# Performance work log

Measured on AMD Instinct MI355X. Metric: run time of the kernel, lower is better.

The kernel has to match this reference:

```python
import jax, jax.numpy as jnp
import numpy as np

EMBED_DIM = 768
NUM_HEADS = 12
HEAD_DIM = EMBED_DIM // NUM_HEADS
BS, SEQ = 2, 2048
NEG_BIG = -1e20  # matches torch masked_fill value


def setup_inputs() -> dict:
    key = jax.random.key(0)
    ks = jax.random.split(key, 8)
    Q = jax.random.normal(ks[0], (BS, SEQ, EMBED_DIM), dtype=jnp.float32)
    K = jax.random.normal(ks[1], (BS, SEQ, EMBED_DIM), dtype=jnp.float32)
    V = jax.random.normal(ks[2], (BS, SEQ, EMBED_DIM), dtype=jnp.float32)
    mask = jax.random.randint(ks[3], (1, 1, SEQ, SEQ), 0, 2, dtype=jnp.int32)
    scale = 1.0 / np.sqrt(EMBED_DIM).astype(np.float32)
    Wq = jax.random.normal(ks[4], (EMBED_DIM, EMBED_DIM), dtype=jnp.float32) * 0.02
    Wk = jax.random.normal(ks[5], (EMBED_DIM, EMBED_DIM), dtype=jnp.float32) * 0.02
    Wv = jax.random.normal(ks[6], (EMBED_DIM, EMBED_DIM), dtype=jnp.float32) * 0.02
    Wo = jax.random.normal(ks[7], (EMBED_DIM, EMBED_DIM), dtype=jnp.float32) * 0.02
    return {"Q": Q, "K": K, "V": V, "mask": mask,
            "Wq": Wq, "Wk": Wk, "Wv": Wv, "Wo": Wo}


def reference(Q, K, V, mask, Wq, Wk, Wv, Wo):
    bs, q_len, D = Q.shape
    H, hd = NUM_HEADS, HEAD_DIM
    # QKV projections (nn.Linear, no bias): x @ W.T
    q = (Q @ Wq.T).reshape(bs, q_len, H, hd)            # nqhd
    k = (K @ Wk.T).reshape(bs, K.shape[1], H, hd)       # nkhd
    v = (V @ Wv.T).reshape(bs, V.shape[1], H, hd)       # nlhd
    # unfused attention, faithful to source (scale by sqrt(embed_dim)!)
    energy = jnp.einsum('nqhd,nkhd->nhqk', q, k)
    energy = jnp.where(mask == 0, jnp.float32(NEG_BIG), energy)
    attn = jax.nn.softmax(energy * (1.0 / jnp.sqrt(jnp.float32(D))), axis=3)
    out = jnp.einsum('nhql,nlhd->nqhd', attn, v).reshape(bs, q_len, H * hd)
    return out @ Wo.T
```

## Files before the change

kernel.cpp:

```cpp
#include <hip/hip_runtime.h>
#include <cmath>

typedef __bf16 bf16x8 __attribute__((ext_vector_type(8)));
typedef float f32x4 __attribute__((ext_vector_type(4)));
typedef unsigned int u32x4 __attribute__((ext_vector_type(4)));

#define SEQ 2048
#define EMBED 768
#define NHEAD 12
#define HDIM 64
#define NTOK 4096
#define NBH 24
#define NSPLIT 2
#define TILES_PER_SPLIT (SEQ / 64 / NSPLIT)
#define SCALE_LOG2 (1.4426950408889634f * 0.036084391824351615f)

__device__ __forceinline__ void gload_lds16(const __bf16* g, __bf16* l) {
  __builtin_amdgcn_global_load_lds(
      (const __attribute__((address_space(1))) void*)g,
      (__attribute__((address_space(3))) void*)l, 16, 0, 0);
}

__device__ __forceinline__ unsigned pack2(float a, float b) {
  unsigned short lo = __builtin_bit_cast(unsigned short, (__bf16)a);
  unsigned short hi = __builtin_bit_cast(unsigned short, (__bf16)b);
  return (unsigned)lo | ((unsigned)hi << 16);
}

__device__ __forceinline__ void phase_barrier() {
  asm volatile("s_waitcnt vmcnt(0)" ::: "memory");
  __builtin_amdgcn_s_barrier();
  __builtin_amdgcn_sched_barrier(0);
}

__global__ __launch_bounds__(256) void cvt_qkv(const float* __restrict__ Q,
                                               const float* __restrict__ K,
                                               const float* __restrict__ V,
                                               __bf16* __restrict__ Qb,
                                               __bf16* __restrict__ Kb,
                                               __bf16* __restrict__ Vb) {
  const float* s = blockIdx.y == 0 ? Q : blockIdx.y == 1 ? K : V;
  __bf16* d = blockIdx.y == 0 ? Qb : blockIdx.y == 1 ? Kb : Vb;
  size_t i = ((size_t)blockIdx.x * 256 + threadIdx.x) * 8;
  float4 a = *(const float4*)(s + i);
  float4 c = *(const float4*)(s + i + 4);
  bf16x8 r;
  r[0] = (__bf16)a.x; r[1] = (__bf16)a.y; r[2] = (__bf16)a.z; r[3] = (__bf16)a.w;
  r[4] = (__bf16)c.x; r[5] = (__bf16)c.y; r[6] = (__bf16)c.z; r[7] = (__bf16)c.w;
  *(bf16x8*)(d + i) = r;
}

__global__ __launch_bounds__(256) void cvt_w(const float* __restrict__ W0,
                                             const float* __restrict__ W1,
                                             const float* __restrict__ W2,
                                             const float* __restrict__ W3,
                                             __bf16* __restrict__ O0,
                                             __bf16* __restrict__ O1,
                                             __bf16* __restrict__ O2,
                                             __bf16* __restrict__ O3) {
  const float* s = blockIdx.y == 0 ? W0 : blockIdx.y == 1 ? W1 : blockIdx.y == 2 ? W2 : W3;
  __bf16* d = blockIdx.y == 0 ? O0 : blockIdx.y == 1 ? O1 : blockIdx.y == 2 ? O2 : O3;
  size_t i = ((size_t)blockIdx.x * 256 + threadIdx.x) * 8;
  float4 a = *(const float4*)(s + i);
  float4 c = *(const float4*)(s + i + 4);
  bf16x8 r;
  r[0] = (__bf16)a.x; r[1] = (__bf16)a.y; r[2] = (__bf16)a.z; r[3] = (__bf16)a.w;
  r[4] = (__bf16)c.x; r[5] = (__bf16)c.y; r[6] = (__bf16)c.z; r[7] = (__bf16)c.w;
  *(bf16x8*)(d + i) = r;
}

__global__ __launch_bounds__(256) void pack_mask_k(const int* __restrict__ mask,
                                                   unsigned long long* __restrict__ bits) {
  int e = blockIdx.x * 256 + threadIdx.x;
  unsigned long long b = __ballot(mask[e] != 0);
  if ((threadIdx.x & 63) == 0) bits[e >> 6] = b;
}

template <int MODE, typename CT>
__device__ __forceinline__ void gemm_body(const __bf16* __restrict__ A,
                                          const __bf16* __restrict__ B,
                                          CT* __restrict__ C, int N, int row0,
                                          int col0, float alpha, __bf16* As,
                                          __bf16* Bs) {
  const int K = EMBED;
  const int NIT = K / 64;
  const int tid = threadIdx.x;
  const int lane = tid & 63;
  const int wave = tid >> 6;
  const int wr = wave >> 1, wc = wave & 1;
  const int l15 = lane & 15, g = lane >> 4;
  f32x4 acc[4][4] = {};

  const int srow = tid >> 3;
  const int scol8 = (tid & 7) ^ (srow & 7);
  const __bf16* aS = A + (size_t)(row0 + srow) * K + scol8 * 8;
  const __bf16* bS = B + (size_t)(col0 + srow) * K + scol8 * 8;
  __bf16* aL = As + wave * 512;
  __bf16* bL = Bs + wave * 512;

  auto stage = [&](int buf, int k0) {
#pragma unroll
    for (int q = 0; q < 4; ++q) {
      gload_lds16(aS + k0 + (size_t)(q * 32) * K, aL + buf * 8192 + q * 2048);
      gload_lds16(bS + k0 + (size_t)(q * 32) * K, bL + buf * 8192 + q * 2048);
    }
  };

  stage(0, 0);
#pragma unroll 2
  for (int it = 0; it < NIT; ++it) {
    const int c = it & 1;
    phase_barrier();
    if (it + 1 < NIT) stage(1 - c, (it + 1) * 64);
    const __bf16* Asc = As + c * 8192;
    const __bf16* Bsc = Bs + c * 8192;
    bf16x8 af[2][4], bfr[2][4];
#pragma unroll
    for (int i = 0; i < 4; ++i) {
      int row = wr * 64 + i * 16 + l15;
#pragma unroll
      for (int kk = 0; kk < 2; ++kk)
        af[kk][i] =
            *(const bf16x8*)(Asc + row * 64 + ((kk * 4 + g) ^ (row & 7)) * 8);
    }
#pragma unroll
    for (int j = 0; j < 4; ++j) {
      int row = wc * 64 + j * 16 + l15;
#pragma unroll
      for (int kk = 0; kk < 2; ++kk)
        bfr[kk][j] =
            *(const bf16x8*)(Bsc + row * 64 + ((kk * 4 + g) ^ (row & 7)) * 8);
    }
    __builtin_amdgcn_s_setprio(1);
#pragma unroll
    for (int kk = 0; kk < 2; ++kk)
#pragma unroll
      for (int i = 0; i < 4; ++i)
#pragma unroll
        for (int j = 0; j < 4; ++j)
          acc[i][j] = __builtin_amdgcn_mfma_f32_16x16x32_bf16(
              af[kk][i], bfr[kk][j], acc[i][j], 0, 0, 0);
    __builtin_amdgcn_s_setprio(0);
  }
#pragma unroll
  for (int i = 0; i < 4; ++i)
#pragma unroll
    for (int j = 0; j < 4; ++j) {
#pragma unroll
      for (int r = 0; r < 4; ++r) {
        float val = alpha * acc[i][j][r];
        int mrow = row0 + wr * 64 + i * 16 + g * 4 + r;
        int ncol = col0 + wc * 64 + j * 16 + l15;
        if (MODE == 0 || MODE == 3) {
          C[(size_t)mrow * N + ncol] = (CT)val;
        } else if (MODE == 1) {
          int tok = mrow, fcol = ncol;
          int h = fcol >> 6, d = fcol & 63;
          int bh = (tok >> 11) * NHEAD + h;
          int t = (tok >> 6) & 31, kk = tok & 63;
          size_t idx = ((size_t)bh * 32 + t) * 4096 +
                       ((((kk >> 4) * 2 + (d >> 5)) * 64 + ((d >> 3) & 3) * 16 +
                         (kk & 15)) *
                            8 +
                        (d & 7));
          C[idx] = (CT)val;
        } else {
          int fr = mrow, tok = ncol;
          int h = fr >> 6, d = fr & 63;
          int dt = d >> 4, l15c = d & 15;
          int bh = (tok >> 11) * NHEAD + h;
          int t = (tok >> 6) & 31, kk = tok & 63;
          int pc = (kk & 32) | ((kk & 12) << 1) | ((kk & 16) >> 2) | (kk & 3);
          int ks = pc >> 5, Gb = (pc >> 3) & 3, e = pc & 7;
          size_t idx = ((size_t)bh * 32 + t) * 4096 +
                       (((ks * 4 + dt) * 64 + Gb * 16 + l15c) * 8 + e);
          C[idx] = (CT)val;
        }
      }
    }
}

__global__ __launch_bounds__(256) void gemm_qkv(
    const __bf16* __restrict__ Qb, const __bf16* __restrict__ Kb,
    const __bf16* __restrict__ Vb, const __bf16* __restrict__ Wqb,
    const __bf16* __restrict__ Wkb, const __bf16* __restrict__ Wvb,
    __bf16* __restrict__ qh, __bf16* __restrict__ khF, __bf16* __restrict__ vTF) {
  __shared__ __align__(16) __bf16 As[2 * 128 * 64];
  __shared__ __align__(16) __bf16 Bs[2 * 128 * 64];
  if (blockIdx.z == 0)
    gemm_body<0, __bf16>(Qb, Wqb, qh, EMBED, blockIdx.x * 128,
                         blockIdx.y * 128, SCALE_LOG2, As, Bs);
  else if (blockIdx.z == 1)
    gemm_body<1, __bf16>(Kb, Wkb, khF, 0, blockIdx.x * 128, blockIdx.y * 128,
                         1.f, As, Bs);
  else
    gemm_body<2, __bf16>(Wvb, Vb, vTF, 0, blockIdx.y * 128, blockIdx.x * 128,
                         1.f, As, Bs);
}

__global__ __launch_bounds__(256) void gemm_out(const __bf16* __restrict__ AO,
                                                const __bf16* __restrict__ Wob,
                                                float* __restrict__ out) {
  __shared__ __align__(16) __bf16 As[2 * 128 * 64];
  __shared__ __align__(16) __bf16 Bs[2 * 128 * 64];
  gemm_body<3, float>(AO, Wob, out, EMBED, blockIdx.x * 128, blockIdx.y * 128,
                      1.f, As, Bs);
}

__global__ __launch_bounds__(256, 4) void flash_attn(
    const __bf16* __restrict__ qh, const __bf16* __restrict__ khF,
    const __bf16* __restrict__ vTF, const unsigned long long* __restrict__ mbits,
    float* __restrict__ Opart, float* __restrict__ lpart) {
  __shared__ __align__(16) __bf16 Ks[2][4096];
  __shared__ __align__(16) __bf16 Vs[2][4096];
  int lin = blockIdx.x + 16 * (blockIdx.y + NBH * blockIdx.z);
  int wid = (lin & 7) * 96 + (lin >> 3);
  int qb = wid & 15;
  int rest = wid >> 4;
  int bh = rest % NBH;
  int z = rest / NBH;

  const int tid = threadIdx.x;
  const int lane = tid & 63, w = tid >> 6;
  const int l15 = lane & 15, G = lane >> 4;
  const int b = bh / NHEAD, h = bh % NHEAD;
  const int qrow0 = qb * 128 + w * 32;

  bf16x8 qf[2][2];
#pragma unroll
  for (int qg = 0; qg < 2; ++qg) {
    const __bf16* qptr =
        qh + ((size_t)b * SEQ + qrow0 + qg * 16 + l15) * EMBED + h * HDIM + G * 8;
    qf[qg][0] = *(const bf16x8*)qptr;
    qf[qg][1] = *(const bf16x8*)(qptr + 32);
  }
  const u32x4 onesr = {0x3F803F80u, 0x3F803F80u, 0x3F803F80u, 0x3F803F80u};
  const bf16x8 ones = __builtin_bit_cast(bf16x8, onesr);

  f32x4 o[2][4] = {};
  f32x4 ol[2] = {};

  const __bf16* ktile =
      khF + ((size_t)bh * 32 + z * TILES_PER_SPLIT) * 4096 + tid * 8;
  const __bf16* vtile =
      vTF + ((size_t)bh * 32 + z * TILES_PER_SPLIT) * 4096 + tid * 8;
  const unsigned long long* mrow0 =
      mbits + (size_t)(qrow0 + l15) * 32 + z * TILES_PER_SPLIT;
  const unsigned long long* mrow1 = mrow0 + 16 * 32;

  gload_lds16(ktile, &Ks[0][0] + w * 512);
  gload_lds16(ktile + 2048, &Ks[0][0] + w * 512 + 2048);
  gload_lds16(vtile, &Vs[0][0] + w * 512);
  gload_lds16(vtile + 2048, &Vs[0][0] + w * 512 + 2048);
  unsigned long long mb0 = mrow0[0], mb1 = mrow1[0];

#pragma unroll 2
  for (int tt = 0; tt < TILES_PER_SPLIT; ++tt) {
    const int c = tt & 1;
    phase_barrier();
    unsigned long long nmb0 = 0, nmb1 = 0;
    if (tt + 1 < TILES_PER_SPLIT) {
      const __bf16* kt = ktile + (size_t)(tt + 1) * 4096;
      const __bf16* vt = vtile + (size_t)(tt + 1) * 4096;
      __bf16* kd = &Ks[1 - c][0] + w * 512;
      __bf16* vd = &Vs[1 - c][0] + w * 512;
      gload_lds16(kt, kd);
      gload_lds16(kt + 2048, kd + 2048);
      gload_lds16(vt, vd);
      gload_lds16(vt + 2048, vd + 2048);
      nmb0 = mrow0[tt + 1];
      nmb1 = mrow1[tt + 1];
    }

    f32x4 s[2][4];
    __builtin_amdgcn_s_setprio(1);
#pragma unroll
    for (int jj = 0; jj < 4; ++jj) {
      bf16x8 kf0 = *(const bf16x8*)(&Ks[c][0] + (jj * 2 + 0) * 512 + lane * 8);
      bf16x8 kf1 = *(const bf16x8*)(&Ks[c][0] + (jj * 2 + 1) * 512 + lane * 8);
#pragma unroll
      for (int qg = 0; qg < 2; ++qg) {
        f32x4 zz = {};
        zz = __builtin_amdgcn_mfma_f32_16x16x32_bf16(kf0, qf[qg][0], zz, 0, 0, 0);
        zz = __builtin_amdgcn_mfma_f32_16x16x32_bf16(kf1, qf[qg][1], zz, 0, 0, 0);
        s[qg][jj] = zz;
      }
    }
    __builtin_amdgcn_s_setprio(0);

    unsigned pfw[2][2][4];
#pragma unroll
    for (int qg = 0; qg < 2; ++qg) {
      unsigned long long mb = qg == 0 ? mb0 : mb1;
      unsigned mlo = ((unsigned)mb) >> (G * 4);
      unsigned mhi = ((unsigned)(mb >> 32)) >> (G * 4);
#pragma unroll
      for (int jj = 0; jj < 4; ++jj) {
        unsigned bits = (jj < 2 ? mlo : mhi) >> ((jj & 1) * 16);
#pragma unroll
        for (int r = 0; r < 4; ++r) {
          float p = __builtin_amdgcn_exp2f(s[qg][jj][r]);
          int sm = ((int)(bits << (31 - r))) >> 31;
          s[qg][jj][r] = __builtin_bit_cast(
              float, __builtin_bit_cast(unsigned, p) & (unsigned)sm);
        }
      }
#pragma unroll
      for (int ks = 0; ks < 2; ++ks) {
        pfw[qg][ks][0] = pack2(s[qg][2 * ks][0], s[qg][2 * ks][1]);
        pfw[qg][ks][1] = pack2(s[qg][2 * ks][2], s[qg][2 * ks][3]);
        pfw[qg][ks][2] = pack2(s[qg][2 * ks + 1][0], s[qg][2 * ks + 1][1]);
        pfw[qg][ks][3] = pack2(s[qg][2 * ks + 1][2], s[qg][2 * ks + 1][3]);
      }
    }
    __builtin_amdgcn_s_setprio(1);
#pragma unroll
    for (int ks = 0; ks < 2; ++ks) {
      u32x4 p0 = {pfw[0][ks][0], pfw[0][ks][1], pfw[0][ks][2], pfw[0][ks][3]};
      u32x4 p1 = {pfw[1][ks][0], pfw[1][ks][1], pfw[1][ks][2], pfw[1][ks][3]};
      bf16x8 pf0 = __builtin_bit_cast(bf16x8, p0);
      bf16x8 pf1 = __builtin_bit_cast(bf16x8, p1);
      ol[0] = __builtin_amdgcn_mfma_f32_16x16x32_bf16(ones, pf0, ol[0], 0, 0, 0);
      ol[1] = __builtin_amdgcn_mfma_f32_16x16x32_bf16(ones, pf1, ol[1], 0, 0, 0);
#pragma unroll
      for (int dt = 0; dt < 4; ++dt) {
        bf16x8 vf = *(const bf16x8*)(&Vs[c][0] + (ks * 4 + dt) * 512 + lane * 8);
        o[0][dt] = __builtin_amdgcn_mfma_f32_16x16x32_bf16(vf, pf0, o[0][dt], 0, 0, 0);
        o[1][dt] = __builtin_amdgcn_mfma_f32_16x16x32_bf16(vf, pf1, o[1][dt], 0, 0, 0);
      }
    }
    __builtin_amdgcn_s_setprio(0);
    mb0 = nmb0;
    mb1 = nmb1;
  }
#pragma unroll
  for (int qg = 0; qg < 2; ++qg) {
    int qrow = qrow0 + qg * 16 + l15;
    size_t obase = (((size_t)z * NBH + bh) * SEQ + qrow) * HDIM;
    f32x4* op = (f32x4*)(Opart + obase);
#pragma unroll
    for (int dt = 0; dt < 4; ++dt) op[dt * 4 + G] = o[qg][dt];
    if (G == 0)
      lpart[((size_t)z * NBH + bh) * SEQ + qrow] = ol[qg][0];
  }
}

__global__ __launch_bounds__(256) void combine(const float* __restrict__ Opart,
                                               const float* __restrict__ lpart,
                                               __bf16* __restrict__ AO) {
  int idx = blockIdx.x * 256 + threadIdx.x;
  int bhq = idx >> 4, dq = idx & 15;
  int bh = bhq >> 11, q = bhq & (SEQ - 1);
  const f32x4* Ov = (const f32x4*)Opart;
  float lsum = 0.f;
  float r0 = 0.f, r1 = 0.f, r2 = 0.f, r3 = 0.f;
#pragma unroll
  for (int s = 0; s < NSPLIT; ++s) {
    lsum += lpart[(size_t)s * NBH * SEQ + bhq];
    f32x4 a = Ov[(size_t)s * NBH * SEQ * 16 + (size_t)bhq * 16 + dq];
    r0 += a[0];
    r1 += a[1];
    r2 += a[2];
    r3 += a[3];
  }
  float inv = 1.f / lsum;
  int bb = bh / NHEAD, hh = bh % NHEAD;
  unsigned* dst =
      (unsigned*)(AO + ((size_t)bb * SEQ + q) * EMBED + hh * HDIM + dq * 4);
  dst[0] = pack2(r0 * inv, r1 * inv);
  dst[1] = pack2(r2 * inv, r3 * inv);
}

extern "C" void kernel_launch(void* const* d_in, const int* in_sizes, int n_in,
                              void* d_out, int out_size, void* d_ws,
                              size_t ws_size, hipStream_t stream) {
  const float* Q = (const float*)d_in[0];
  const float* K = (const float*)d_in[1];
  const float* V = (const float*)d_in[2];
  const int* mask = (const int*)d_in[3];
  const float* Wq = (const float*)d_in[4];
  const float* Wk = (const float*)d_in[5];
  const float* Wv = (const float*)d_in[6];
  const float* Wo = (const float*)d_in[7];
  float* out = (float*)d_out;

  char* ws = (char*)d_ws;
  const size_t ACT = (size_t)NTOK * EMBED * 2;
  const size_t WMT = (size_t)EMBED * EMBED * 2;
  const size_t OPART_B = (size_t)NSPLIT * NBH * SEQ * HDIM * 4;

  float* Opart = (float*)ws;
  __bf16* Qb = (__bf16*)ws;
  __bf16* Kb = (__bf16*)(ws + ACT);
  __bf16* Vb = (__bf16*)(ws + 2 * ACT);
  __bf16* Wqb = (__bf16*)(ws + 3 * ACT);
  __bf16* Wkb = (__bf16*)(ws + 3 * ACT + WMT);
  __bf16* Wvb = (__bf16*)(ws + 3 * ACT + 2 * WMT);
  size_t off = OPART_B;
  auto alloc = [&](size_t bytes) {
    char* p = ws + off;
    off += (bytes + 255) & ~(size_t)255;
    return p;
  };
  __bf16* Wob = (__bf16*)alloc(WMT);
  __bf16* qh = (__bf16*)alloc(ACT);
  __bf16* khF = (__bf16*)alloc(ACT);
  __bf16* vTF = (__bf16*)alloc(ACT);
  __bf16* AO = (__bf16*)alloc(ACT);
  unsigned long long* mbits =
      (unsigned long long*)alloc((size_t)SEQ * (SEQ / 64) * 8);
  float* lpart = (float*)alloc((size_t)NSPLIT * NBH * SEQ * 4);

  cvt_qkv<<<dim3(NTOK * EMBED / 2048, 3), 256, 0, stream>>>(Q, K, V, Qb, Kb, Vb);
  cvt_w<<<dim3(EMBED * EMBED / 2048, 4), 256, 0, stream>>>(Wq, Wk, Wv, Wo, Wqb,
                                                           Wkb, Wvb, Wob);
  pack_mask_k<<<dim3(SEQ * SEQ / 256), 256, 0, stream>>>(mask, mbits);
  gemm_qkv<<<dim3(NTOK / 128, EMBED / 128, 3), 256, 0, stream>>>(
      Qb, Kb, Vb, Wqb, Wkb, Wvb, qh, khF, vTF);
  flash_attn<<<dim3(SEQ / 128, NBH, NSPLIT), 256, 0, stream>>>(qh, khF, vTF,
                                                               mbits, Opart,
                                                               lpart);
  combine<<<dim3(NBH * SEQ * 16 / 256), 256, 0, stream>>>(Opart, lpart, AO);
  gemm_out<<<dim3(NTOK / 128, EMBED / 128), 256, 0, stream>>>(AO, Wob, out);
  (void)in_sizes; (void)n_in; (void)out_size; (void)ws_size;
}
```

Before: 116.8 us.

## Merge prep kernels into one launch and simplify GEMM to single-buffered K=32 tiles

The three preprocessing kernels (activation cast, weight cast, mask bit-packing) become one `prep` kernel that dispatches on block index. This removes two kernel launches and their gaps. The shared GEMM body drops its double-buffered, XOR-swizzled 64-wide K staging. It now uses a single 32-wide K buffer with two block barriers per step, which also cuts LDS use per block. In exchange, global loads no longer overlap with MFMA work, and the unswizzled LDS reads may cause bank conflicts.

New measurement: 127.3 us. +9.0%, slower.

```diff
diff --git a/kernel.cpp b/kernel.cpp
--- a/kernel.cpp
+++ b/kernel.cpp
@@ -33,47 +33,47 @@
   __builtin_amdgcn_sched_barrier(0);
 }
 
-__global__ __launch_bounds__(256) void cvt_qkv(const float* __restrict__ Q,
-                                               const float* __restrict__ K,
-                                               const float* __restrict__ V,
-                                               __bf16* __restrict__ Qb,
-                                               __bf16* __restrict__ Kb,
-                                               __bf16* __restrict__ Vb) {
-  const float* s = blockIdx.y == 0 ? Q : blockIdx.y == 1 ? K : V;
-  __bf16* d = blockIdx.y == 0 ? Qb : blockIdx.y == 1 ? Kb : Vb;
-  size_t i = ((size_t)blockIdx.x * 256 + threadIdx.x) * 8;
-  float4 a = *(const float4*)(s + i);
-  float4 c = *(const float4*)(s + i + 4);
-  bf16x8 r;
-  r[0] = (__bf16)a.x; r[1] = (__bf16)a.y; r[2] = (__bf16)a.z; r[3] = (__bf16)a.w;
-  r[4] = (__bf16)c.x; r[5] = (__bf16)c.y; r[6] = (__bf16)c.z; r[7] = (__bf16)c.w;
-  *(bf16x8*)(d + i) = r;
-}
-
-__global__ __launch_bounds__(256) void cvt_w(const float* __restrict__ W0,
-                                             const float* __restrict__ W1,
-                                             const float* __restrict__ W2,
-                                             const float* __restrict__ W3,
-                                             __bf16* __restrict__ O0,
-                                             __bf16* __restrict__ O1,
-                                             __bf16* __restrict__ O2,
-                                             __bf16* __restrict__ O3) {
-  const float* s = blockIdx.y == 0 ? W0 : blockIdx.y == 1 ? W1 : blockIdx.y == 2 ? W2 : W3;
-  __bf16* d = blockIdx.y == 0 ? O0 : blockIdx.y == 1 ? O1 : blockIdx.y == 2 ? O2 : O3;
-  size_t i = ((size_t)blockIdx.x * 256 + threadIdx.x) * 8;
-  float4 a = *(const float4*)(s + i);
-  float4 c = *(const float4*)(s + i + 4);
-  bf16x8 r;
-  r[0] = (__bf16)a.x; r[1] = (__bf16)a.y; r[2] = (__bf16)a.z; r[3] = (__bf16)a.w;
-  r[4] = (__bf16)c.x; r[5] = (__bf16)c.y; r[6] = (__bf16)c.z; r[7] = (__bf16)c.w;
-  *(bf16x8*)(d + i) = r;
-}
-
-__global__ __launch_bounds__(256) void pack_mask_k(const int* __restrict__ mask,
-                                                   unsigned long long* __restrict__ bits) {
-  int e = blockIdx.x * 256 + threadIdx.x;
-  unsigned long long b = __ballot(mask[e] != 0);
-  if ((threadIdx.x & 63) == 0) bits[e >> 6] = b;
+#define NB_A (NTOK * EMBED / 2048)
+#define NB_W (EMBED * EMBED / 2048)
+#define NB_M (SEQ * SEQ / 256)
+__global__ __launch_bounds__(256) void prep(
+    const float* __restrict__ Q, const float* __restrict__ K,
+    const float* __restrict__ V, const float* __restrict__ Wq,
+    const float* __restrict__ Wk, const float* __restrict__ Wv,
+    const float* __restrict__ Wo, const int* __restrict__ mask,
+    __bf16* __restrict__ Qb, __bf16* __restrict__ Kb, __bf16* __restrict__ Vb,
+    __bf16* __restrict__ Wqb, __bf16* __restrict__ Wkb,
+    __bf16* __restrict__ Wvb, __bf16* __restrict__ Wob,
+    unsigned long long* __restrict__ bits) {
+  int bid = blockIdx.x;
+  if (bid < 3 * NB_A + 4 * NB_W) {
+    const float* s;
+    __bf16* d;
+    int sub;
+    if (bid < 3 * NB_A) {
+      int which = bid / NB_A;
+      sub = bid % NB_A;
+      s = which == 0 ? Q : which == 1 ? K : V;
+      d = which == 0 ? Qb : which == 1 ? Kb : Vb;
+    } else {
+      int r = bid - 3 * NB_A;
+      int which = r / NB_W;
+      sub = r % NB_W;
+      s = which == 0 ? Wq : which == 1 ? Wk : which == 2 ? Wv : Wo;
+      d = which == 0 ? Wqb : which == 1 ? Wkb : which == 2 ? Wvb : Wob;
+    }
+    size_t i = ((size_t)sub * 256 + threadIdx.x) * 8;
+    float4 a = *(const float4*)(s + i);
+    float4 c = *(const float4*)(s + i + 4);
+    bf16x8 r;
+    r[0] = (__bf16)a.x; r[1] = (__bf16)a.y; r[2] = (__bf16)a.z; r[3] = (__bf16)a.w;
+    r[4] = (__bf16)c.x; r[5] = (__bf16)c.y; r[6] = (__bf16)c.z; r[7] = (__bf16)c.w;
+    *(bf16x8*)(d + i) = r;
+  } else {
+    int e = (bid - (3 * NB_A + 4 * NB_W)) * 256 + threadIdx.x;
+    unsigned long long b = __ballot(mask[e] != 0);
+    if ((threadIdx.x & 63) == 0) bits[e >> 6] = b;
+  }
 }
 
 template <int MODE, typename CT>
@@ -83,7 +83,6 @@
                                           int col0, float alpha, __bf16* As,
                                           __bf16* Bs) {
   const int K = EMBED;
-  const int NIT = K / 64;
   const int tid = threadIdx.x;
   const int lane = tid & 63;
   const int wave = tid >> 6;
@@ -91,55 +90,32 @@
   const int l15 = lane & 15, g = lane >> 4;
   f32x4 acc[4][4] = {};
 
-  const int srow = tid >> 3;
-  const int scol8 = (tid & 7) ^ (srow & 7);
-  const __bf16* aS = A + (size_t)(row0 + srow) * K + scol8 * 8;
-  const __bf16* bS = B + (size_t)(col0 + srow) * K + scol8 * 8;
+  const __bf16* aS = A + (size_t)(row0 + (tid >> 2)) * K + (tid & 3) * 8;
+  const __bf16* bS = B + (size_t)(col0 + (tid >> 2)) * K + (tid & 3) * 8;
   __bf16* aL = As + wave * 512;
   __bf16* bL = Bs + wave * 512;
 
-  auto stage = [&](int buf, int k0) {
-#pragma unroll
-    for (int q = 0; q < 4; ++q) {
-      gload_lds16(aS + k0 + (size_t)(q * 32) * K, aL + buf * 8192 + q * 2048);
-      gload_lds16(bS + k0 + (size_t)(q * 32) * K, bL + buf * 8192 + q * 2048);
-    }
-  };
-
-  stage(0, 0);
-#pragma unroll 2
-  for (int it = 0; it < NIT; ++it) {
-    const int c = it & 1;
-    phase_barrier();
-    if (it + 1 < NIT) stage(1 - c, (it + 1) * 64);
-    const __bf16* Asc = As + c * 8192;
-    const __bf16* Bsc = Bs + c * 8192;
-    bf16x8 af[2][4], bfr[2][4];
-#pragma unroll
-    for (int i = 0; i < 4; ++i) {
-      int row = wr * 64 + i * 16 + l15;
-#pragma unroll
-      for (int kk = 0; kk < 2; ++kk)
-        af[kk][i] =
-            *(const bf16x8*)(Asc + row * 64 + ((kk * 4 + g) ^ (row & 7)) * 8);
-    }
-#pragma unroll
-    for (int j = 0; j < 4; ++j) {
-      int row = wc * 64 + j * 16 + l15;
-#pragma unroll
-      for (int kk = 0; kk < 2; ++kk)
-        bfr[kk][j] =
-            *(const bf16x8*)(Bsc + row * 64 + ((kk * 4 + g) ^ (row & 7)) * 8);
-    }
+  for (int k0 = 0; k0 < K; k0 += 32) {
+    __syncthreads();
+    gload_lds16(aS + k0, aL);
+    gload_lds16(aS + k0 + (size_t)64 * K, aL + 2048);
+    gload_lds16(bS + k0, bL);
+    gload_lds16(bS + k0 + (size_t)64 * K, bL + 2048);
+    __syncthreads();
+    bf16x8 af[4], bfr[4];
+#pragma unroll
+    for (int i = 0; i < 4; ++i)
+      af[i] = *(const bf16x8*)(As + (wr * 64 + i * 16 + l15) * 32 + g * 8);
+#pragma unroll
+    for (int j = 0; j < 4; ++j)
+      bfr[j] = *(const bf16x8*)(Bs + (wc * 64 + j * 16 + l15) * 32 + g * 8);
     __builtin_amdgcn_s_setprio(1);
 #pragma unroll
-    for (int kk = 0; kk < 2; ++kk)
-#pragma unroll
-      for (int i = 0; i < 4; ++i)
-#pragma unroll
-        for (int j = 0; j < 4; ++j)
-          acc[i][j] = __builtin_amdgcn_mfma_f32_16x16x32_bf16(
-              af[kk][i], bfr[kk][j], acc[i][j], 0, 0, 0);
+    for (int i = 0; i < 4; ++i)
+#pragma unroll
+      for (int j = 0; j < 4; ++j)
+        acc[i][j] = __builtin_amdgcn_mfma_f32_16x16x32_bf16(af[i], bfr[j],
+                                                            acc[i][j], 0, 0, 0);
     __builtin_amdgcn_s_setprio(0);
   }
 #pragma unroll
@@ -185,8 +161,8 @@
     const __bf16* __restrict__ Vb, const __bf16* __restrict__ Wqb,
     const __bf16* __restrict__ Wkb, const __bf16* __restrict__ Wvb,
     __bf16* __restrict__ qh, __bf16* __restrict__ khF, __bf16* __restrict__ vTF) {
-  __shared__ __align__(16) __bf16 As[2 * 128 * 64];
-  __shared__ __align__(16) __bf16 Bs[2 * 128 * 64];
+  __shared__ __align__(16) __bf16 As[128 * 32];
+  __shared__ __align__(16) __bf16 Bs[128 * 32];
   if (blockIdx.z == 0)
     gemm_body<0, __bf16>(Qb, Wqb, qh, EMBED, blockIdx.x * 128,
                          blockIdx.y * 128, SCALE_LOG2, As, Bs);
@@ -201,8 +177,8 @@
 __global__ __launch_bounds__(256) void gemm_out(const __bf16* __restrict__ AO,
                                                 const __bf16* __restrict__ Wob,
                                                 float* __restrict__ out) {
-  __shared__ __align__(16) __bf16 As[2 * 128 * 64];
-  __shared__ __align__(16) __bf16 Bs[2 * 128 * 64];
+  __shared__ __align__(16) __bf16 As[128 * 32];
+  __shared__ __align__(16) __bf16 Bs[128 * 32];
   gemm_body<3, float>(AO, Wob, out, EMBED, blockIdx.x * 128, blockIdx.y * 128,
                       1.f, As, Bs);
 }
@@ -411,10 +387,8 @@
       (unsigned long long*)alloc((size_t)SEQ * (SEQ / 64) * 8);
   float* lpart = (float*)alloc((size_t)NSPLIT * NBH * SEQ * 4);
 
-  cvt_qkv<<<dim3(NTOK * EMBED / 2048, 3), 256, 0, stream>>>(Q, K, V, Qb, Kb, Vb);
-  cvt_w<<<dim3(EMBED * EMBED / 2048, 4), 256, 0, stream>>>(Wq, Wk, Wv, Wo, Wqb,
-                                                           Wkb, Wvb, Wob);
-  pack_mask_k<<<dim3(SEQ * SEQ / 256), 256, 0, stream>>>(mask, mbits);
+  prep<<<dim3(3 * NB_A + 4 * NB_W + NB_M), 256, 0, stream>>>(
+      Q, K, V, Wq, Wk, Wv, Wo, mask, Qb, Kb, Vb, Wqb, Wkb, Wvb, Wob, mbits);
   gemm_qkv<<<dim3(NTOK / 128, EMBED / 128, 3), 256, 0, stream>>>(
       Qb, Kb, Vb, Wqb, Wkb, Wvb, qh, khF, vTF);
   flash_attn<<<dim3(SEQ / 128, NBH, NSPLIT), 256, 0, stream>>>(qh, khF, vTF,
```
